# Optimization experiments

Hardware: AMD Instinct MI355X
Metric: run time of the kernel (lower is better)

The kernel has to match this reference:

```python
import jax, jax.numpy as jnp
import numpy as np
import math

NUM_HEADS = 32
NUM_KV_HEADS = 8
HEAD_DIM = 128
SCALE = 1.0 / math.sqrt(128.0)
MAX_SEQLEN = 1152  # static max sequence length for padding
CU = [0, 1024, 1920, 3072, 4096]  # cumulative seq lens, batch=4
NUM_SLOTS = 8192  # 32 blocks * block_size 256


def setup_inputs() -> dict:
    key = jax.random.key(0)
    k0, k1, k2 = jax.random.split(key, 3)
    T = CU[-1]
    q = jax.random.normal(k0, (T, NUM_HEADS, HEAD_DIM), jnp.float32)
    k = jax.random.normal(k1, (T, NUM_KV_HEADS, HEAD_DIM), jnp.float32)
    v = jax.random.normal(k2, (T, NUM_KV_HEADS, HEAD_DIM), jnp.float32)
    k_cache = jnp.zeros((NUM_SLOTS, NUM_KV_HEADS, HEAD_DIM), jnp.float32)
    v_cache = jnp.zeros((NUM_SLOTS, NUM_KV_HEADS, HEAD_DIM), jnp.float32)
    cu_seqlens = jnp.array(CU, dtype=jnp.int32)
    slot_mapping = jnp.arange(T, dtype=jnp.int32)
    return {"q": q, "k": k, "v": v, "k_cache": k_cache, "v_cache": v_cache,
            "cu_seqlens": cu_seqlens, "slot_mapping": slot_mapping}


def _store_kv(key, value, k_cache, v_cache, slot_mapping):
    # scatter new K/V into paged cache; slot == -1 means skip
    valid = slot_mapping >= 0
    safe = jnp.where(valid, slot_mapping, 0)
    k_cache = k_cache.at[safe].set(
        jnp.where(valid[:, None, None], key, k_cache[safe]), mode='drop')
    v_cache = v_cache.at[safe].set(
        jnp.where(valid[:, None, None], value, v_cache[safe]), mode='drop')
    return k_cache, v_cache


def _prefill_attention(q, k, v, cu_seqlens):
    T = q.shape[0]
    B = cu_seqlens.shape[0] - 1
    groups = NUM_HEADS // NUM_KV_HEADS
    k = jnp.repeat(k, groups, axis=1)  # GQA expand -> [T, H, D]
    v = jnp.repeat(v, groups, axis=1)

    lens = cu_seqlens[1:] - cu_seqlens[:-1]            # [B]
    s = jnp.arange(MAX_SEQLEN)
    idx = cu_seqlens[:-1][:, None] + s[None, :]        # [B, S] packed token index
    valid = s[None, :] < lens[:, None]                 # [B, S]
    idx_safe = jnp.where(valid, idx, 0)

    # pack -> padded [B, S, H, D], zeroing pad positions
    qp = jnp.where(valid[..., None, None], q[idx_safe], 0.0)
    kp = jnp.where(valid[..., None, None], k[idx_safe], 0.0)
    vp = jnp.where(valid[..., None, None], v[idx_safe], 0.0)

    scores = jnp.einsum('bqhd,bkhd->bhqk', qp, kp) * SCALE  # [B, H, S, S]
    causal = s[:, None] >= s[None, :]                       # [S, S]
    mask = (causal[None, :, :] & valid[:, :, None] & valid[:, None, :])[:, None, :, :]
    scores = jnp.where(mask, scores, jnp.finfo(scores.dtype).min)
    attn = jax.nn.softmax(scores, axis=-1)
    outp = jnp.einsum('bhqk,bkhd->bqhd', attn, vp)          # [B, S, H, D]

    # unpack padded -> packed [T, H, D]
    tok = jnp.arange(T)
    seq_id = jnp.searchsorted(cu_seqlens, tok, side='right') - 1
    pos = tok - cu_seqlens[seq_id]
    return outp[seq_id, pos]


def reference(q, k, v, k_cache, v_cache, cu_seqlens, slot_mapping):
    k_cache, v_cache = _store_kv(k, v, k_cache, v_cache, slot_mapping)
    out = _prefill_attention(q, k, v, cu_seqlens)
    return out, k_cache, v_cache
```

## Files before the change

kernel.cpp:

```cpp
#include <hip/hip_runtime.h>
#include <hip/hip_bf16.h>

#define T_TOT   4096
#define NH      32
#define NKV     8
#define GQ      4
#define DHEAD   128
#define NSLOTS  8192
#define QB      64
#define QW      32
#define KVB     64
#define ATT_SCALE 0.088388347648318447f

typedef __attribute__((ext_vector_type(8))) short bf16x8;
typedef __attribute__((ext_vector_type(4))) float f32x4;

__device__ __forceinline__ unsigned short f2bf(float f) {
    union { float f; unsigned u; } x; x.f = f;
    unsigned r = x.u + 0x7fffu + ((x.u >> 16) & 1u);
    return (unsigned short)(r >> 16);
}

__device__ __forceinline__ unsigned long long pack4bf(float a, float b, float c, float d) {
    unsigned lo = (unsigned)f2bf(a) | ((unsigned)f2bf(b) << 16);
    unsigned hi = (unsigned)f2bf(c) | ((unsigned)f2bf(d) << 16);
    return (unsigned long long)lo | ((unsigned long long)hi << 32);
}


__global__ __launch_bounds__(256) void copy_cache(const float4* __restrict__ kc,
                                                  const float4* __restrict__ vc,
                                                  float4* __restrict__ kco,
                                                  float4* __restrict__ vco) {
    int idx = blockIdx.x * 256 + threadIdx.x;
    kco[idx] = kc[idx];
    vco[idx] = vc[idx];
}

__global__ __launch_bounds__(256) void scatter_kv(const float4* __restrict__ k,
                                                  const float4* __restrict__ v,
                                                  const int* __restrict__ slot_map,
                                                  float4* __restrict__ kco,
                                                  float4* __restrict__ vco) {
    int idx = blockIdx.x * 256 + threadIdx.x;
    int tok = idx >> 8;
    int j   = idx & 255;
    int slot = slot_map[tok];
    if (slot >= 0 && slot < NSLOTS) {
        size_t dst = (size_t)slot * 256 + j;
        kco[dst] = k[idx];
        vco[dst] = v[idx];
    }
}


__global__ __launch_bounds__(512, 2) void attn_kernel(const float* __restrict__ qg,
                                                      const float* __restrict__ kg,
                                                      const float* __restrict__ vg,
                                                      const int* __restrict__ cu,
                                                      float* __restrict__ outg)
{
    __shared__ __align__(16) char Klds[KVB * 256];
    __shared__ __align__(16) char Vt[DHEAD * 128];
    __shared__ __align__(16) char Plds[8][QW * 128];

    const int tid  = threadIdx.x;
    const int wave = tid >> 6;
    const int lane = tid & 63;
    const int q16  = lane & 15;
    const int grp  = lane >> 4;
    const int kvh  = blockIdx.y;
    const int head = kvh * GQ + (wave >> 1);
    const int tok0 = blockIdx.x * QB;
    const int qw0  = tok0 + (wave & 1) * QW;

    int seq_start = 0;
    #pragma unroll
    for (int b = 0; b < 4; ++b) {
        int c0 = cu[b], c1 = cu[b + 1];
        if (tok0 >= c0 && tok0 < c1) seq_start = c0;
    }
    const int p0  = tok0 - seq_start;
    const int pw0 = p0 + (wave & 1) * QW;
    const int ntiles = p0 / KVB + 1;

    bf16x8 qf[2][4];
    {
        const float* qp = qg + ((size_t)(qw0 + q16) * NH + head) * DHEAD + grp * 8;
        #pragma unroll
        for (int qt = 0; qt < 2; ++qt) {
            #pragma unroll
            for (int c = 0; c < 4; ++c) {
                const float* p = qp + (size_t)qt * 16 * NH * DHEAD + c * 32;
                float4 a = *(const float4*)(p);
                float4 b = *(const float4*)(p + 4);
                union { bf16x8 v; unsigned long long q[2]; } u;
                u.q[0] = pack4bf(a.x, a.y, a.z, a.w);
                u.q[1] = pack4bf(b.x, b.y, b.z, b.w);
                qf[qt][c] = u.v;
            }
        }
    }

    f32x4 oacc[2][8];
    #pragma unroll
    for (int qt = 0; qt < 2; ++qt)
        #pragma unroll
        for (int n = 0; n < 8; ++n) oacc[qt][n] = (f32x4){0.f, 0.f, 0.f, 0.f};
    float mrow[2][4], lrow[2][4];
    #pragma unroll
    for (int qt = 0; qt < 2; ++qt)
        #pragma unroll
        for (int r = 0; r < 4; ++r) { mrow[qt][r] = -1e30f; lrow[qt][r] = 0.f; }

    char* Pw = Plds[wave];

    for (int t = 0; t < ntiles; ++t) {
        const int k0 = t * KVB;
        __syncthreads();
        #pragma unroll
        for (int i = 0; i < 4; ++i) {
            int idx = tid + i * 512;
            int key = idx >> 5;
            int d4  = idx & 31;
            float4 kv4 = *(const float4*)(kg +
                ((size_t)(seq_start + k0 + key) * NKV + kvh) * DHEAD + d4 * 4);
            *(unsigned long long*)(Klds + key * 256 + ((d4 * 8) ^ ((key & 7) << 4))) =
                pack4bf(kv4.x, kv4.y, kv4.z, kv4.w);
        }
        #pragma unroll
        for (int i = 0; i < 4; ++i) {
            int job = tid + i * 512;
            int kq  = job >> 7;
            int d   = job & 127;
            const float* vp = vg +
                ((size_t)(seq_start + k0 + kq * 4) * NKV + kvh) * DHEAD + d;
            float c0 = vp[0];
            float c1 = vp[NKV * DHEAD];
            float c2 = vp[2 * NKV * DHEAD];
            float c3 = vp[3 * NKV * DHEAD];
            *(unsigned long long*)(Vt + d * 128 + ((kq * 8) ^ ((d & 15) << 3))) =
                pack4bf(c0, c1, c2, c3);
        }
        __syncthreads();

        float sv[2][4][4];
        const bool lastt = (t == ntiles - 1);
        #pragma unroll
        for (int ktile = 0; ktile < 4; ++ktile) {
            f32x4 sacc0 = (f32x4){0.f, 0.f, 0.f, 0.f};
            f32x4 sacc1 = (f32x4){0.f, 0.f, 0.f, 0.f};
            int row = ktile * 16 + q16;
            #pragma unroll
            for (int c = 0; c < 4; ++c) {
                bf16x8 kf = *(bf16x8*)(Klds + row * 256 +
                                       ((c * 64 + grp * 16) ^ ((row & 7) << 4)));
                sacc0 = __builtin_amdgcn_mfma_f32_16x16x32_bf16(qf[0][c], kf, sacc0, 0, 0, 0);
                sacc1 = __builtin_amdgcn_mfma_f32_16x16x32_bf16(qf[1][c], kf, sacc1, 0, 0, 0);
            }
            if (lastt) {
                int kpos = k0 + ktile * 16 + q16;
                #pragma unroll
                for (int r = 0; r < 4; ++r) {
                    int qp0 = pw0 + grp * 4 + r;
                    sv[0][ktile][r] = (kpos <= qp0)      ? sacc0[r] * ATT_SCALE : -1e30f;
                    sv[1][ktile][r] = (kpos <= qp0 + 16) ? sacc1[r] * ATT_SCALE : -1e30f;
                }
            } else {
                #pragma unroll
                for (int r = 0; r < 4; ++r) {
                    sv[0][ktile][r] = sacc0[r] * ATT_SCALE;
                    sv[1][ktile][r] = sacc1[r] * ATT_SCALE;
                }
            }
        }

        #pragma unroll
        for (int qt = 0; qt < 2; ++qt) {
            #pragma unroll
            for (int r = 0; r < 4; ++r) {
                float tm = fmaxf(fmaxf(sv[qt][0][r], sv[qt][1][r]),
                                 fmaxf(sv[qt][2][r], sv[qt][3][r]));
                #pragma unroll
                for (int mm = 1; mm < 16; mm <<= 1) tm = fmaxf(tm, __shfl_xor(tm, mm));
                float newm = fmaxf(mrow[qt][r], tm);
                float scal = __expf(mrow[qt][r] - newm);
                float ps = 0.f;
                int qrow = qt * 16 + grp * 4 + r;
                #pragma unroll
                for (int ktile = 0; ktile < 4; ++ktile) {
                    float e = __expf(sv[qt][ktile][r] - newm);
                    ps += e;
                    int key = ktile * 16 + q16;
                    *(unsigned short*)(Pw + qrow * 128 +
                        ((key * 2) ^ ((qrow & 7) << 4))) = f2bf(e);
                }
                #pragma unroll
                for (int mm = 1; mm < 16; mm <<= 1) ps += __shfl_xor(ps, mm);
                lrow[qt][r] = lrow[qt][r] * scal + ps;
                mrow[qt][r] = newm;
                #pragma unroll
                for (int n = 0; n < 8; ++n) oacc[qt][n][r] *= scal;
            }
        }

        #pragma unroll
        for (int kt = 0; kt < 2; ++kt) {
            bf16x8 pf[2];
            #pragma unroll
            for (int qt = 0; qt < 2; ++qt) {
                int qrow = qt * 16 + q16;
                pf[qt] = *(bf16x8*)(Pw + qrow * 128 +
                                    ((kt * 64 + grp * 16) ^ ((qrow & 7) << 4)));
            }
            #pragma unroll
            for (int n = 0; n < 8; ++n) {
                int d = n * 16 + q16;
                int kq0 = kt * 8 + grp * 2;
                union { bf16x8 v8; unsigned long long q[2]; } uv;
                uv.q[0] = *(unsigned long long*)(Vt + d * 128 + ((kq0 * 8) ^ ((d & 15) << 3)));
                uv.q[1] = *(unsigned long long*)(Vt + d * 128 + (((kq0 + 1) * 8) ^ ((d & 15) << 3)));
                oacc[0][n] = __builtin_amdgcn_mfma_f32_16x16x32_bf16(pf[0], uv.v8, oacc[0][n], 0, 0, 0);
                oacc[1][n] = __builtin_amdgcn_mfma_f32_16x16x32_bf16(pf[1], uv.v8, oacc[1][n], 0, 0, 0);
            }
        }
    }

    #pragma unroll
    for (int qt = 0; qt < 2; ++qt) {
        #pragma unroll
        for (int r = 0; r < 4; ++r) {
            float inv = 1.0f / lrow[qt][r];
            float* op = outg + ((size_t)(qw0 + qt * 16 + grp * 4 + r) * NH + head) * DHEAD;
            #pragma unroll
            for (int n = 0; n < 8; ++n) op[n * 16 + q16] = oacc[qt][n][r] * inv;
        }
    }
}


extern "C" void kernel_launch(void* const* d_in, const int* in_sizes, int n_in,
                              void* d_out, int out_size, void* d_ws, size_t ws_size,
                              hipStream_t stream) {
    const float* q  = (const float*)d_in[0];
    const float* k  = (const float*)d_in[1];
    const float* v  = (const float*)d_in[2];
    const float* kc = (const float*)d_in[3];
    const float* vc = (const float*)d_in[4];
    const int* cu   = (const int*)d_in[5];
    const int* slot = (const int*)d_in[6];

    float* out    = (float*)d_out;
    float* kc_out = out + (size_t)T_TOT * NH * DHEAD;
    float* vc_out = kc_out + (size_t)NSLOTS * NKV * DHEAD;

    copy_cache<<<dim3((NSLOTS * NKV * DHEAD / 4) / 256), dim3(256), 0, stream>>>(
        (const float4*)kc, (const float4*)vc, (float4*)kc_out, (float4*)vc_out);
    scatter_kv<<<dim3((T_TOT * NKV * DHEAD / 4) / 256), dim3(256), 0, stream>>>(
        (const float4*)k, (const float4*)v, slot, (float4*)kc_out, (float4*)vc_out);

    attn_kernel<<<dim3(T_TOT / QB, NKV), dim3(512), 0, stream>>>(q, k, v, cu, out);
}
```

Measured before the change: 424.0 us.

## Pre-convert K/V to bf16 tiles, async LDS loads, lazy rescale, reorder blocks

A new prep kernel converts K and V once to bf16 in the swizzled LDS tile layout and writes them into the cache output buffers as scratch space. The attention kernel then copies whole tiles into LDS with global_load_lds instead of converting fp32 data on every block. Other changes: blocks are mapped through a longest-first work order table, the online softmax rescales only when the running max grows by more than 8, and setprio is raised around the MFMA sections. The cache copy and scatter now run after attention so they overwrite the scratch data, and the lazy rescale changes the numerics slightly.

```diff
diff --git a/kernel.cpp b/kernel.cpp
--- a/kernel.cpp
+++ b/kernel.cpp
@@ -10,6 +10,7 @@
 #define QB      64
 #define QW      32
 #define KVB     64
+#define NTILES  (T_TOT / KVB)
 #define ATT_SCALE 0.088388347648318447f
 
 typedef __attribute__((ext_vector_type(8))) short bf16x8;
@@ -26,6 +27,20 @@
     unsigned hi = (unsigned)f2bf(c) | ((unsigned)f2bf(d) << 16);
     return (unsigned long long)lo | ((unsigned long long)hi << 32);
 }
+
+__device__ __forceinline__ void gload16(const char* g, char* l) {
+    __builtin_amdgcn_global_load_lds(
+        (const __attribute__((address_space(1))) void*)g,
+        (__attribute__((address_space(3))) void*)l,
+        16, 0, 0);
+}
+
+__constant__ unsigned char QORD[64] = {
+    47,46,15,45,63,14,44,62,13,29,43,61,12,28,42,60,
+    11,27,41,59,10,26,40,58, 9,25,39,57, 8,24,38,56,
+     7,23,37,55, 6,22,36,54, 5,21,35,53, 4,20,34,52,
+     3,19,33,51, 2,18,32,50, 1,17,31,49, 0,16,30,48
+};
 
 
 __global__ __launch_bounds__(256) void copy_cache(const float4* __restrict__ kc,
@@ -54,9 +69,39 @@
 }
 
 
+__global__ __launch_bounds__(256) void prep_kv(const float* __restrict__ kg,
+                                               const float* __restrict__ vg,
+                                               char* __restrict__ kbf,
+                                               char* __restrict__ vbf) {
+    const int tile = blockIdx.x;
+    const int kvh  = blockIdx.y;
+    const int tid  = threadIdx.x;
+    char* kt = kbf + (((size_t)kvh * NTILES + tile) << 14);
+    char* vt = vbf + (((size_t)kvh * NTILES + tile) << 14);
+    #pragma unroll
+    for (int it = 0; it < 8; ++it) {
+        int idx = tid + it * 256;
+        int key = idx >> 5, d4 = idx & 31;
+        float4 x = *(const float4*)(kg +
+            ((size_t)(tile * 64 + key) * NKV + kvh) * DHEAD + d4 * 4);
+        *(unsigned long long*)(kt + key * 256 + ((d4 * 8) ^ ((key & 7) << 4))) =
+            pack4bf(x.x, x.y, x.z, x.w);
+    }
+    #pragma unroll
+    for (int it = 0; it < 8; ++it) {
+        int job = tid + it * 256;
+        int kq = job >> 7, d = job & 127;
+        const float* vp = vg +
+            ((size_t)(tile * 64 + kq * 4) * NKV + kvh) * DHEAD + d;
+        *(unsigned long long*)(vt + d * 128 + ((kq * 8) ^ ((d & 15) << 3))) =
+            pack4bf(vp[0], vp[NKV * DHEAD], vp[2 * NKV * DHEAD], vp[3 * NKV * DHEAD]);
+    }
+}
+
+
 __global__ __launch_bounds__(512, 2) void attn_kernel(const float* __restrict__ qg,
-                                                      const float* __restrict__ kg,
-                                                      const float* __restrict__ vg,
+                                                      const char* __restrict__ kbf,
+                                                      const char* __restrict__ vbf,
                                                       const int* __restrict__ cu,
                                                       float* __restrict__ outg)
 {
@@ -69,9 +114,11 @@
     const int lane = tid & 63;
     const int q16  = lane & 15;
     const int grp  = lane >> 4;
-    const int kvh  = blockIdx.y;
+    const int bid  = blockIdx.x;
+    const int qblk = QORD[bid >> 3];
+    const int kvh  = bid & 7;
     const int head = kvh * GQ + (wave >> 1);
-    const int tok0 = blockIdx.x * QB;
+    const int tok0 = qblk * QB;
     const int qw0  = tok0 + (wave & 1) * QW;
 
     int seq_start = 0;
@@ -83,6 +130,7 @@
     const int p0  = tok0 - seq_start;
     const int pw0 = p0 + (wave & 1) * QW;
     const int ntiles = p0 / KVB + 1;
+    const int tile0 = seq_start >> 6;
 
     bf16x8 qf[2][4];
     {
@@ -114,38 +162,23 @@
         for (int r = 0; r < 4; ++r) { mrow[qt][r] = -1e30f; lrow[qt][r] = 0.f; }
 
     char* Pw = Plds[wave];
+    const int wbase = wave * 2048;
 
     for (int t = 0; t < ntiles; ++t) {
         const int k0 = t * KVB;
+        const char* gK = kbf + (((size_t)kvh * NTILES + tile0 + t) << 14);
+        const char* gV = vbf + (((size_t)kvh * NTILES + tile0 + t) << 14);
         __syncthreads();
         #pragma unroll
-        for (int i = 0; i < 4; ++i) {
-            int idx = tid + i * 512;
-            int key = idx >> 5;
-            int d4  = idx & 31;
-            float4 kv4 = *(const float4*)(kg +
-                ((size_t)(seq_start + k0 + key) * NKV + kvh) * DHEAD + d4 * 4);
-            *(unsigned long long*)(Klds + key * 256 + ((d4 * 8) ^ ((key & 7) << 4))) =
-                pack4bf(kv4.x, kv4.y, kv4.z, kv4.w);
-        }
-        #pragma unroll
-        for (int i = 0; i < 4; ++i) {
-            int job = tid + i * 512;
-            int kq  = job >> 7;
-            int d   = job & 127;
-            const float* vp = vg +
-                ((size_t)(seq_start + k0 + kq * 4) * NKV + kvh) * DHEAD + d;
-            float c0 = vp[0];
-            float c1 = vp[NKV * DHEAD];
-            float c2 = vp[2 * NKV * DHEAD];
-            float c3 = vp[3 * NKV * DHEAD];
-            *(unsigned long long*)(Vt + d * 128 + ((kq * 8) ^ ((d & 15) << 3))) =
-                pack4bf(c0, c1, c2, c3);
+        for (int i = 0; i < 2; ++i) {
+            gload16(gK + wbase + i * 1024 + lane * 16, Klds + wbase + i * 1024);
+            gload16(gV + wbase + i * 1024 + lane * 16, Vt   + wbase + i * 1024);
         }
         __syncthreads();
 
         float sv[2][4][4];
         const bool lastt = (t == ntiles - 1);
+        __builtin_amdgcn_s_setprio(1);
         #pragma unroll
         for (int ktile = 0; ktile < 4; ++ktile) {
             f32x4 sacc0 = (f32x4){0.f, 0.f, 0.f, 0.f};
@@ -174,6 +207,7 @@
                 }
             }
         }
+        __builtin_amdgcn_s_setprio(0);
 
         #pragma unroll
         for (int qt = 0; qt < 2; ++qt) {
@@ -183,27 +217,31 @@
                                  fmaxf(sv[qt][2][r], sv[qt][3][r]));
                 #pragma unroll
                 for (int mm = 1; mm < 16; mm <<= 1) tm = fmaxf(tm, __shfl_xor(tm, mm));
-                float newm = fmaxf(mrow[qt][r], tm);
-                float scal = __expf(mrow[qt][r] - newm);
+                if (__any(tm > mrow[qt][r] + 8.0f)) {
+                    float newm = fmaxf(tm, mrow[qt][r]);
+                    float scal = __expf(mrow[qt][r] - newm);
+                    mrow[qt][r] = newm;
+                    lrow[qt][r] *= scal;
+                    #pragma unroll
+                    for (int n = 0; n < 8; ++n) oacc[qt][n][r] *= scal;
+                }
+                float m = mrow[qt][r];
                 float ps = 0.f;
                 int qrow = qt * 16 + grp * 4 + r;
                 #pragma unroll
-                for (int ktile = 0; ktile < 4; ++ktile) {
-                    float e = __expf(sv[qt][ktile][r] - newm);
+                for (int kt2 = 0; kt2 < 4; ++kt2) {
+                    float e = __expf(sv[qt][kt2][r] - m);
                     ps += e;
-                    int key = ktile * 16 + q16;
                     *(unsigned short*)(Pw + qrow * 128 +
-                        ((key * 2) ^ ((qrow & 7) << 4))) = f2bf(e);
+                        (((kt2 * 16 + q16) * 2) ^ ((qrow & 7) << 4))) = f2bf(e);
                 }
                 #pragma unroll
                 for (int mm = 1; mm < 16; mm <<= 1) ps += __shfl_xor(ps, mm);
-                lrow[qt][r] = lrow[qt][r] * scal + ps;
-                mrow[qt][r] = newm;
-                #pragma unroll
-                for (int n = 0; n < 8; ++n) oacc[qt][n][r] *= scal;
-            }
-        }
-
+                lrow[qt][r] += ps;
+            }
+        }
+
+        __builtin_amdgcn_s_setprio(1);
         #pragma unroll
         for (int kt = 0; kt < 2; ++kt) {
             bf16x8 pf[2];
@@ -224,6 +262,7 @@
                 oacc[1][n] = __builtin_amdgcn_mfma_f32_16x16x32_bf16(pf[1], uv.v8, oacc[1][n], 0, 0, 0);
             }
         }
+        __builtin_amdgcn_s_setprio(0);
     }
 
     #pragma unroll
@@ -254,10 +293,14 @@
     float* kc_out = out + (size_t)T_TOT * NH * DHEAD;
     float* vc_out = kc_out + (size_t)NSLOTS * NKV * DHEAD;
 
+    char* kbf = (char*)kc_out;
+    char* vbf = (char*)vc_out;
+
+    prep_kv<<<dim3(NTILES, NKV), dim3(256), 0, stream>>>(k, v, kbf, vbf);
+    attn_kernel<<<dim3(512), dim3(512), 0, stream>>>(q, kbf, vbf, cu, out);
+
     copy_cache<<<dim3((NSLOTS * NKV * DHEAD / 4) / 256), dim3(256), 0, stream>>>(
         (const float4*)kc, (const float4*)vc, (float4*)kc_out, (float4*)vc_out);
     scatter_kv<<<dim3((T_TOT * NKV * DHEAD / 4) / 256), dim3(256), 0, stream>>>(
         (const float4*)k, (const float4*)v, slot, (float4*)kc_out, (float4*)vc_out);
-
-    attn_kernel<<<dim3(T_TOT / QB, NKV), dim3(512), 0, stream>>>(q, k, v, cu, out);
-}
+}
```

Result: faster. 353.5 us (-16.6%).
